# Kernel tuning notes

Hardware: AMD Instinct MI355X
Metric: run time of the kernel (lower is better)

Reference implementation:

```python
import jax, jax.numpy as jnp
import numpy as np

B, N, INNER, OUT, DEPTH = 128, 128, 40, 512, 2
F = INNER + 1  # last channel is the bond/adjacency channel


def setup_inputs() -> dict:
    key = jax.random.key(0)
    k0, k1, k2, k3, k4 = jax.random.split(key, 5)
    return {
        "graph": jax.random.normal(k0, (B, N, N, F), dtype=jnp.float32),
        # build() inits: identity tiled for W_inner, uniform*0.05 for W_output, zero biases.
        # We add small noise so the reference exercises nondegenerate paths.
        "W_inner": jnp.tile(jnp.eye(INNER, dtype=jnp.float32)[None], (DEPTH + 1, 1, 1))
        + 0.05 * jax.random.normal(k1, (DEPTH + 1, INNER, INNER), dtype=jnp.float32),
        "b_inner": 0.05 * jax.random.normal(k2, (DEPTH + 1, 1, INNER), dtype=jnp.float32),
        "W_output": 0.05 * jax.random.normal(k3, (DEPTH + 1, INNER, OUT), dtype=jnp.float32),
        "b_output": 0.05 * jax.random.normal(k4, (DEPTH + 1, 1, OUT), dtype=jnp.float32),
    }


def reference(graph, W_inner, b_inner, W_output, b_output):
    depth = W_inner.shape[0] - 1

    def fp_contrib(attrs, d):
        # softmax over fingerprint dim, summed over atoms -> (OUT,)
        logits = attrs[:, :-1] @ W_output[d] + b_output[d, 0]
        return jax.nn.softmax(logits, axis=-1).sum(axis=0)

    def single(g):  # g: (N, N, F) for one molecule
        n = g.shape[0]
        # attributes[i, f] = g[i, i, f]  (per-atom diagonal extraction)
        attrs = jnp.diagonal(g, axis1=0, axis2=1).T  # (N, F)
        bonds = g[:, :, -1]                          # (N, N)
        boa = bonds + jnp.eye(n, dtype=g.dtype)      # bonds_or_atoms
        fp = fp_contrib(attrs, 0)
        cur = g
        for d in range(1, depth + 1):
            # sum over neighbors j: pre[i, f] = sum_j cur[i, j, f], drop bond channel
            pre = cur[:, :, :-1].sum(axis=1)                     # (N, INNER)
            new_core = pre @ W_inner[d] + b_inner[d, 0]          # linear inner activation
            new_attrs = jnp.concatenate([new_core, attrs[:, -1:]], axis=1)  # (N, F)
            # new_graph[i,j,f] = cur[i,j,f] + boa[j,i] * (new_attrs[i,f] - attrs[i,f])
            cur = cur + boa.T[:, :, None] * (new_attrs - attrs)[:, None, :]
            attrs = new_attrs
            fp = fp + fp_contrib(attrs, d)
        return fp  # (OUT,)

    return jax.vmap(single)(graph)  # (B, OUT)
```

## Files before the change

kernel.cpp:

```cpp
#include <hip/hip_runtime.h>

#define Bn 128
#define Nn 128
#define Fn 41
#define INNERn 40
#define OUTn 512
#define SLAB (Nn*Fn)

__global__ __launch_bounds__(256) void k1_reduce(
    const float* __restrict__ g, float* __restrict__ X0,
    float* __restrict__ pre1, float* __restrict__ S)
{
    __shared__ float lds[SLAB];
    __shared__ float part[6*INNERn];
    const int t = threadIdx.x;
    const int blk = blockIdx.x;
    const int b = blk >> 7;
    const int i = blk & 127;

    const float4* __restrict__ src = (const float4*)(g + (size_t)blk * SLAB);
    float4* dst = (float4*)lds;
    #pragma unroll
    for (int it = 0; it < 5; ++it) dst[t + 256*it] = src[t + 256*it];
    if (t < (SLAB/4 - 1280)) dst[1280 + t] = src[1280 + t];
    __syncthreads();

    if (t < 240) {
        const int grp = t / 40;
        const int f = t - grp*40;
        float s = 0.f;
        for (int j = grp; j < Nn; j += 6) s += lds[j*Fn + f];
        part[grp*INNERn + f] = s;
    }
    if (t < 128) {
        float v = lds[t*Fn + 40] + ((t == i) ? 1.f : 0.f);
        atomicAdd(&S[b*Nn + t], v);
    }
    if (t < 40) {
        X0[(size_t)blk*INNERn + t] = lds[i*Fn + t];
    }
    __syncthreads();
    if (t < 40) {
        float s = part[t] + part[INNERn + t] + part[2*INNERn + t]
                + part[3*INNERn + t] + part[4*INNERn + t] + part[5*INNERn + t];
        pre1[(size_t)blk*INNERn + t] = s;
    }
}

__global__ __launch_bounds__(256) void k2_chain(
    const float* __restrict__ pre1, const float* __restrict__ X0,
    const float* __restrict__ S, const float* __restrict__ Wi,
    const float* __restrict__ bi, float* __restrict__ X1, float* __restrict__ X2)
{
    __shared__ float W1[INNERn*INNERn], W2[INNERn*INNERn];
    __shared__ float A[32*INNERn];
    __shared__ float T[32*INNERn];
    __shared__ float Sv[32];
    const int t = threadIdx.x;
    const size_t row0 = (size_t)blockIdx.x * 32;

    for (int idx = t; idx < INNERn*INNERn; idx += 256) {
        W1[idx] = Wi[INNERn*INNERn + idx];
        W2[idx] = Wi[2*INNERn*INNERn + idx];
    }
    for (int idx = t; idx < 32*INNERn; idx += 256) {
        A[idx] = pre1[row0*INNERn + idx];
        T[idx] = X0[row0*INNERn + idx];
    }
    if (t < 32) Sv[t] = S[row0 + t];
    __syncthreads();

    float c1[5];
    #pragma unroll
    for (int p = 0; p < 5; ++p) {
        int idx = t + 256*p;
        int r = idx / INNERn, c = idx - r*INNERn;
        float acc = bi[INNERn + c];
        for (int k = 0; k < INNERn; ++k) acc = fmaf(A[r*INNERn + k], W1[k*INNERn + c], acc);
        c1[p] = acc;
    }
    __syncthreads();
    #pragma unroll
    for (int p = 0; p < 5; ++p) {
        int idx = t + 256*p;
        int r = idx / INNERn;
        X1[row0*INNERn + idx] = c1[p];
        A[idx] = A[idx] + Sv[r] * (c1[p] - T[idx]);
    }
    __syncthreads();
    #pragma unroll
    for (int p = 0; p < 5; ++p) {
        int idx = t + 256*p;
        int r = idx / INNERn, c = idx - r*INNERn;
        float acc = bi[2*INNERn + c];
        for (int k = 0; k < INNERn; ++k) acc = fmaf(A[r*INNERn + k], W2[k*INNERn + c], acc);
        X2[row0*INNERn + idx] = acc;
    }
}

__global__ __launch_bounds__(256) void k3_softmax(
    const float* __restrict__ X, const float* __restrict__ Wo,
    const float* __restrict__ bo_g, float* __restrict__ out)
{
    __shared__ float lx[32*INNERn];
    __shared__ float lacc[OUTn];
    const int t = threadIdx.x;
    const int lane = t & 63;
    const int w = t >> 6;
    const int bx = blockIdx.x;
    const int d = bx >> 9;
    const int rem = bx & 511;
    const int b = rem >> 2;
    const int chunk = rem & 3;

    const float* __restrict__ Xb = X + (((size_t)d*Bn + b)*Nn + chunk*32)*INNERn;
    for (int idx = t; idx < 32*INNERn; idx += 256) lx[idx] = Xb[idx];
    for (int idx = t; idx < OUTn; idx += 256) lacc[idx] = 0.f;
    __syncthreads();

    const float* __restrict__ W = Wo + (size_t)d*INNERn*OUTn;
    float acc[8][8];
    #pragma unroll
    for (int r = 0; r < 8; ++r)
        #pragma unroll
        for (int u = 0; u < 8; ++u) acc[r][u] = 0.f;

    for (int k = 0; k < INNERn; ++k) {
        float wv[8];
        #pragma unroll
        for (int u = 0; u < 8; ++u) wv[u] = W[k*OUTn + lane + 64*u];
        #pragma unroll
        for (int r = 0; r < 8; ++r) {
            float a = lx[(w*8 + r)*INNERn + k];
            #pragma unroll
            for (int u = 0; u < 8; ++u) acc[r][u] = fmaf(a, wv[u], acc[r][u]);
        }
    }

    float bv[8];
    #pragma unroll
    for (int u = 0; u < 8; ++u) bv[u] = bo_g[d*OUTn + lane + 64*u];
    float colacc[8];
    #pragma unroll
    for (int u = 0; u < 8; ++u) colacc[u] = 0.f;

    #pragma unroll
    for (int r = 0; r < 8; ++r) {
        float lg[8];
        float m = -3.4e38f;
        #pragma unroll
        for (int u = 0; u < 8; ++u) { lg[u] = acc[r][u] + bv[u]; m = fmaxf(m, lg[u]); }
        #pragma unroll
        for (int off = 32; off > 0; off >>= 1) m = fmaxf(m, __shfl_xor(m, off));
        float s = 0.f, e[8];
        #pragma unroll
        for (int u = 0; u < 8; ++u) { e[u] = __expf(lg[u] - m); s += e[u]; }
        #pragma unroll
        for (int off = 32; off > 0; off >>= 1) s += __shfl_xor(s, off);
        float inv = 1.f / s;
        #pragma unroll
        for (int u = 0; u < 8; ++u) colacc[u] = fmaf(e[u], inv, colacc[u]);
    }

    #pragma unroll
    for (int u = 0; u < 8; ++u) atomicAdd(&lacc[lane + 64*u], colacc[u]);
    __syncthreads();
    for (int idx = t; idx < OUTn; idx += 256) atomicAdd(&out[(size_t)b*OUTn + idx], lacc[idx]);
}

extern "C" void kernel_launch(void* const* d_in, const int* in_sizes, int n_in,
                              void* d_out, int out_size, void* d_ws, size_t ws_size,
                              hipStream_t stream) {
    const float* g        = (const float*)d_in[0];
    const float* W_inner  = (const float*)d_in[1];
    const float* b_inner  = (const float*)d_in[2];
    const float* W_output = (const float*)d_in[3];
    const float* b_output = (const float*)d_in[4];
    float* out = (float*)d_out;
    float* ws  = (float*)d_ws;

    const size_t nBN = (size_t)Bn * Nn;
    float* X    = ws;
    float* X0   = X;
    float* X1   = X + nBN * INNERn;
    float* X2   = X + 2 * nBN * INNERn;
    float* pre1 = X + 3 * nBN * INNERn;
    float* S    = pre1 + nBN * INNERn;

    hipMemsetAsync(S, 0, nBN * sizeof(float), stream);
    hipMemsetAsync(d_out, 0, (size_t)out_size * sizeof(float), stream);

    k1_reduce<<<Bn*Nn, 256, 0, stream>>>(g, X0, pre1, S);
    k2_chain<<<(Bn*Nn)/32, 256, 0, stream>>>(pre1, X0, S, W_inner, b_inner, X1, X2);
    k3_softmax<<<3*Bn*4, 256, 0, stream>>>(X, W_output, b_output, out);
}
```

Baseline: 521.2 us.

## Vectorize softmax weight loads, use per-wave LDS partials, halve k2 tile rows

k3 now has each lane own 8 contiguous output columns, so weight and bias loads become float4 reads. The shared-memory atomicAdd reduction is replaced by per-wave partial arrays that are summed before the global atomics. k2 processes 16 rows per block instead of 32, giving more blocks at the cost of reloading the weight matrices more often, and k1 writes X0 straight from global memory. The k1 stage, which reads the whole 344 MB graph, is still bandwidth-bound, and these changes mostly touch the smaller kernels.

```diff
diff --git a/kernel.cpp b/kernel.cpp
--- a/kernel.cpp
+++ b/kernel.cpp
@@ -18,6 +18,10 @@
     const int b = blk >> 7;
     const int i = blk & 127;
 
+    if (t < 40) {
+        X0[(size_t)blk*INNERn + t] = g[(size_t)blk*SLAB + i*Fn + t];
+    }
+
     const float4* __restrict__ src = (const float4*)(g + (size_t)blk * SLAB);
     float4* dst = (float4*)lds;
     #pragma unroll
@@ -29,15 +33,13 @@
         const int grp = t / 40;
         const int f = t - grp*40;
         float s = 0.f;
+        #pragma unroll 4
         for (int j = grp; j < Nn; j += 6) s += lds[j*Fn + f];
         part[grp*INNERn + f] = s;
     }
     if (t < 128) {
         float v = lds[t*Fn + 40] + ((t == i) ? 1.f : 0.f);
         atomicAdd(&S[b*Nn + t], v);
-    }
-    if (t < 40) {
-        X0[(size_t)blk*INNERn + t] = lds[i*Fn + t];
     }
     __syncthreads();
     if (t < 40) {
@@ -53,48 +55,56 @@
     const float* __restrict__ bi, float* __restrict__ X1, float* __restrict__ X2)
 {
     __shared__ float W1[INNERn*INNERn], W2[INNERn*INNERn];
-    __shared__ float A[32*INNERn];
-    __shared__ float T[32*INNERn];
-    __shared__ float Sv[32];
+    __shared__ float A[16*INNERn];
+    __shared__ float T[16*INNERn];
+    __shared__ float Sv[16];
     const int t = threadIdx.x;
-    const size_t row0 = (size_t)blockIdx.x * 32;
+    const size_t row0 = (size_t)blockIdx.x * 16;
 
     for (int idx = t; idx < INNERn*INNERn; idx += 256) {
         W1[idx] = Wi[INNERn*INNERn + idx];
         W2[idx] = Wi[2*INNERn*INNERn + idx];
     }
-    for (int idx = t; idx < 32*INNERn; idx += 256) {
+    for (int idx = t; idx < 16*INNERn; idx += 256) {
         A[idx] = pre1[row0*INNERn + idx];
         T[idx] = X0[row0*INNERn + idx];
     }
-    if (t < 32) Sv[t] = S[row0 + t];
-    __syncthreads();
-
-    float c1[5];
-    #pragma unroll
-    for (int p = 0; p < 5; ++p) {
+    if (t < 16) Sv[t] = S[row0 + t];
+    __syncthreads();
+
+    float c1[3];
+    #pragma unroll
+    for (int p = 0; p < 3; ++p) {
         int idx = t + 256*p;
-        int r = idx / INNERn, c = idx - r*INNERn;
-        float acc = bi[INNERn + c];
-        for (int k = 0; k < INNERn; ++k) acc = fmaf(A[r*INNERn + k], W1[k*INNERn + c], acc);
-        c1[p] = acc;
-    }
-    __syncthreads();
-    #pragma unroll
-    for (int p = 0; p < 5; ++p) {
+        if (idx < 16*INNERn) {
+            int r = idx / INNERn, c = idx - r*INNERn;
+            float acc = bi[INNERn + c];
+            #pragma unroll 4
+            for (int k = 0; k < INNERn; ++k) acc = fmaf(A[r*INNERn + k], W1[k*INNERn + c], acc);
+            c1[p] = acc;
+        }
+    }
+    __syncthreads();
+    #pragma unroll
+    for (int p = 0; p < 3; ++p) {
         int idx = t + 256*p;
-        int r = idx / INNERn;
-        X1[row0*INNERn + idx] = c1[p];
-        A[idx] = A[idx] + Sv[r] * (c1[p] - T[idx]);
-    }
-    __syncthreads();
-    #pragma unroll
-    for (int p = 0; p < 5; ++p) {
+        if (idx < 16*INNERn) {
+            int r = idx / INNERn;
+            X1[row0*INNERn + idx] = c1[p];
+            A[idx] = A[idx] + Sv[r] * (c1[p] - T[idx]);
+        }
+    }
+    __syncthreads();
+    #pragma unroll
+    for (int p = 0; p < 3; ++p) {
         int idx = t + 256*p;
-        int r = idx / INNERn, c = idx - r*INNERn;
-        float acc = bi[2*INNERn + c];
-        for (int k = 0; k < INNERn; ++k) acc = fmaf(A[r*INNERn + k], W2[k*INNERn + c], acc);
-        X2[row0*INNERn + idx] = acc;
+        if (idx < 16*INNERn) {
+            int r = idx / INNERn, c = idx - r*INNERn;
+            float acc = bi[2*INNERn + c];
+            #pragma unroll 4
+            for (int k = 0; k < INNERn; ++k) acc = fmaf(A[r*INNERn + k], W2[k*INNERn + c], acc);
+            X2[row0*INNERn + idx] = acc;
+        }
     }
 }
 
@@ -103,7 +113,7 @@
     const float* __restrict__ bo_g, float* __restrict__ out)
 {
     __shared__ float lx[32*INNERn];
-    __shared__ float lacc[OUTn];
+    __shared__ float lacc4[4*OUTn];
     const int t = threadIdx.x;
     const int lane = t & 63;
     const int w = t >> 6;
@@ -115,10 +125,9 @@
 
     const float* __restrict__ Xb = X + (((size_t)d*Bn + b)*Nn + chunk*32)*INNERn;
     for (int idx = t; idx < 32*INNERn; idx += 256) lx[idx] = Xb[idx];
-    for (int idx = t; idx < OUTn; idx += 256) lacc[idx] = 0.f;
-    __syncthreads();
-
-    const float* __restrict__ W = Wo + (size_t)d*INNERn*OUTn;
+    __syncthreads();
+
+    const float* __restrict__ W = Wo + (size_t)d*INNERn*OUTn + lane*8;
     float acc[8][8];
     #pragma unroll
     for (int r = 0; r < 8; ++r)
@@ -126,9 +135,10 @@
         for (int u = 0; u < 8; ++u) acc[r][u] = 0.f;
 
     for (int k = 0; k < INNERn; ++k) {
-        float wv[8];
-        #pragma unroll
-        for (int u = 0; u < 8; ++u) wv[u] = W[k*OUTn + lane + 64*u];
+        const float4* __restrict__ wp = (const float4*)(W + k*OUTn);
+        float4 w0 = wp[0];
+        float4 w1 = wp[1];
+        float wv[8] = {w0.x, w0.y, w0.z, w0.w, w1.x, w1.y, w1.z, w1.w};
         #pragma unroll
         for (int r = 0; r < 8; ++r) {
             float a = lx[(w*8 + r)*INNERn + k];
@@ -137,9 +147,10 @@
         }
     }
 
-    float bv[8];
-    #pragma unroll
-    for (int u = 0; u < 8; ++u) bv[u] = bo_g[d*OUTn + lane + 64*u];
+    const float4* __restrict__ bp = (const float4*)(bo_g + d*OUTn + lane*8);
+    float4 b0 = bp[0];
+    float4 b1 = bp[1];
+    float bv[8] = {b0.x, b0.y, b0.z, b0.w, b1.x, b1.y, b1.z, b1.w};
     float colacc[8];
     #pragma unroll
     for (int u = 0; u < 8; ++u) colacc[u] = 0.f;
@@ -163,9 +174,12 @@
     }
 
     #pragma unroll
-    for (int u = 0; u < 8; ++u) atomicAdd(&lacc[lane + 64*u], colacc[u]);
-    __syncthreads();
-    for (int idx = t; idx < OUTn; idx += 256) atomicAdd(&out[(size_t)b*OUTn + idx], lacc[idx]);
+    for (int u = 0; u < 8; ++u) lacc4[w*OUTn + lane*8 + u] = colacc[u];
+    __syncthreads();
+    for (int idx = t; idx < OUTn; idx += 256) {
+        float s = lacc4[idx] + lacc4[OUTn + idx] + lacc4[2*OUTn + idx] + lacc4[3*OUTn + idx];
+        atomicAdd(&out[(size_t)b*OUTn + idx], s);
+    }
 }
 
 extern "C" void kernel_launch(void* const* d_in, const int* in_sizes, int n_in,
@@ -191,6 +205,6 @@
     hipMemsetAsync(d_out, 0, (size_t)out_size * sizeof(float), stream);
 
     k1_reduce<<<Bn*Nn, 256, 0, stream>>>(g, X0, pre1, S);
-    k2_chain<<<(Bn*Nn)/32, 256, 0, stream>>>(pre1, X0, S, W_inner, b_inner, X1, X2);
+    k2_chain<<<(Bn*Nn)/16, 256, 0, stream>>>(pre1, X0, S, W_inner, b_inner, X1, X2);
     k3_softmax<<<3*Bn*4, 256, 0, stream>>>(X, W_output, b_output, out);
 }
```

Result: faster. 507.9 us (-2.5%).
